# Optimization experiments

Hardware: AMD Instinct MI355X
Metric: run time of the kernel (lower is better)

The kernel has to match this reference:

```python
import jax, jax.numpy as jnp
import numpy as np

N_NODES = 50000
N_EDGES = 800000
HID = 64
OUT = 64
REL = 5


def setup_inputs() -> dict:
    key = jax.random.key(0)
    ks = jax.random.split(key, 9)
    s_in = 1.0 / np.sqrt(HID)
    return {
        "contagion_risk": jax.random.normal(ks[0], (N_NODES, HID), jnp.float32),
        "edge_weight": jax.random.uniform(ks[1], (N_EDGES,), jnp.float32),
        # torch Linear weights stored transposed as [in, out] so y = x @ W + b
        "W_in_w": jax.random.uniform(ks[2], (HID, HID), jnp.float32, -s_in, s_in),
        "W_in_b": jax.random.uniform(ks[3], (HID,), jnp.float32, -s_in, s_in),
        "W_rel": jax.random.uniform(ks[4], (REL, HID, HID), jnp.float32, -s_in, s_in),
        "W_out_w": jax.random.uniform(ks[5], (HID, OUT), jnp.float32, -s_in, s_in),
        "W_out_b": jax.random.uniform(ks[6], (OUT,), jnp.float32, -s_in, s_in),
        "edge_index": jax.random.randint(ks[7], (2, N_EDGES), 0, N_NODES, jnp.int64 if jax.config.jax_enable_x64 else jnp.int32),
        "edge_type": jax.random.randint(ks[8], (N_EDGES,), 0, REL, jnp.int32),
        "num_nodes": N_NODES,
    }


def _dan_forward(contagion_risk, W_in_w, W_in_b, W_rel, W_out_w, W_out_b,
                 edge_index, edge_type, num_nodes):
    row, col = edge_index[0], edge_index[1]  # dst, src
    x = contagion_risk @ W_in_w + W_in_b                       # [N, H]
    x_j = x[col]                                               # [E, H] gather

    # gcn_norm (no self loops, unit edge weights): deg over col
    ones = jnp.ones(col.shape[0], x.dtype)
    deg = jax.ops.segment_sum(ones, col, num_segments=num_nodes)
    dis = jnp.where(deg > 0, jax.lax.rsqrt(jnp.maximum(deg, 1.0)), 0.0)
    norm_w = (dis[row] * dis[col])[:, None]                    # [E, 1]
    msg_gcn = jax.ops.segment_sum(x_j * norm_w, row, num_segments=num_nodes)

    # per-relation masked GEMM (grouped GEMM over REL relation types)
    res = jnp.zeros_like(x_j)
    for i in range(W_rel.shape[0]):
        mask = (edge_type == i)[:, None]
        res = res + jnp.where(mask, x_j @ W_rel[i], 0.0)

    # segment softmax over destination-node groups (per feature channel)
    seg_max = jax.ops.segment_max(res, row, num_segments=num_nodes)
    e = jnp.exp(res - seg_max[row])
    seg_sum = jax.ops.segment_sum(e, row, num_segments=num_nodes)
    weig = e / (seg_sum[row] + 1e-16)

    msg = jax.ops.segment_sum(res * weig, row, num_segments=num_nodes)
    out = (msg_gcn + 0.5 * jax.nn.relu(msg)) @ W_out_w + W_out_b
    return out


def reference(contagion_risk, edge_weight, W_in_w, W_in_b, W_rel, W_out_w, W_out_b,
              edge_index, edge_type, num_nodes):
    # edge_weight is accepted by the original forward but never used
    return _dan_forward(contagion_risk, W_in_w, W_in_b, W_rel, W_out_w, W_out_b,
                        edge_index, edge_type, num_nodes)
```

## Files before the change

kernel.cpp:

```cpp
#include <hip/hip_runtime.h>
#include <hip/hip_bf16.h>

#define HID 64
#define REL 5
#define EPB 4096
#define BKT 256

typedef short bf16x8 __attribute__((ext_vector_type(8)));
typedef float f32x4 __attribute__((ext_vector_type(4)));

__device__ __forceinline__ float bf2f(unsigned short u) {
    return __uint_as_float(((unsigned)u) << 16);
}
__device__ __forceinline__ unsigned short f2bf(float f) {
    __hip_bfloat16 h = (__hip_bfloat16)f;
    return *(unsigned short*)&h;
}
__device__ __forceinline__ void dec_edge(const int* __restrict__ ei, int i64,
                                         int E, int e, int& r, int& c) {
    if (i64) { r = ei[2 * e]; c = ei[2 * (E + e)]; }
    else     { r = ei[e];     c = ei[E + e]; }
}

__global__ void k_detect(const unsigned short* __restrict__ wb,
                         const int* __restrict__ ei, int* flags) {
    int lane = threadIdx.x;
    bool big = (lane < 32) ? (fabsf(bf2f(wb[2 * lane])) > 0.26f) : false;
    unsigned long long b1 = __ballot(big);
    bool odd_nz = (ei[2 * lane + 1] != 0);
    unsigned long long b2 = __ballot(odd_nz);
    if (lane == 0) {
        flags[0] = (b1 != 0ull) ? 1 : 0;
        flags[1] = (b2 == 0ull) ? 1 : 0;
    }
}

__global__ void k_pack(const void* Win, const void* bin, const void* Wr,
                       const void* Wout, const void* bout,
                       unsigned short* __restrict__ Bpk,
                       float* __restrict__ binf, float* __restrict__ boutf,
                       const int* __restrict__ flags) {
    int f = flags[0];
    int gid = blockIdx.x * 256 + threadIdx.x;
    if (gid < 7 * 2 * 4 * 64) {
        int lane = gid & 63;
        int nt = (gid >> 6) & 3;
        int ks = (gid >> 8) & 1;
        int mat = gid >> 9;
        int q = lane >> 4, n = nt * 16 + (lane & 15);
#pragma unroll
        for (int j = 0; j < 8; j++) {
            int k = ks * 32 + q * 8 + j;
            int idx = k * 64 + n;
            float val;
            if (mat == 0)
                val = f ? ((const float*)Win)[idx] : bf2f(((const unsigned short*)Win)[idx]);
            else if (mat <= 5) {
                int ii = (mat - 1) * 4096 + idx;
                val = f ? ((const float*)Wr)[ii] : bf2f(((const unsigned short*)Wr)[ii]);
            } else
                val = f ? ((const float*)Wout)[idx] : bf2f(((const unsigned short*)Wout)[idx]);
            Bpk[(size_t)gid * 8 + j] = f2bf(val);
        }
    }
    if (gid < 64)
        binf[gid] = f ? ((const float*)bin)[gid] : bf2f(((const unsigned short*)bin)[gid]);
    else if (gid >= 64 && gid < 128) {
        int i = gid - 64;
        boutf[i] = f ? ((const float*)bout)[i] : bf2f(((const unsigned short*)bout)[i]);
    }
}

__global__ void k_p1a(const int* __restrict__ ei, const int* __restrict__ flags,
                      int* __restrict__ hist, int E, int NB, int nblk) {
    extern __shared__ int lh[];
    int tid = threadIdx.x, blk = blockIdx.x;
    for (int i = tid; i < 2 * NB; i += 256) lh[i] = 0;
    __syncthreads();
    int i64 = flags[1];
#pragma unroll
    for (int k = 0; k < EPB / 256; k++) {
        int e = blk * EPB + k * 256 + tid;
        if (e < E) {
            int r, c;
            dec_edge(ei, i64, E, e, r, c);
            atomicAdd(&lh[r >> 8], 1);
            atomicAdd(&lh[NB + (c >> 8)], 1);
        }
    }
    __syncthreads();
    int NBn = NB * nblk;
    for (int i = tid; i < NB; i += 256) {
        hist[i * nblk + blk] = lh[i];
        hist[NBn + i * nblk + blk] = lh[NB + i];
    }
}

__global__ void s_blk(const int* __restrict__ v, int* __restrict__ bsum, int M) {
    __shared__ int red[256];
    int t = threadIdx.x;
    int i0 = blockIdx.x * 1024 + t * 4;
    int s = 0;
#pragma unroll
    for (int j = 0; j < 4; j++) { int i = i0 + j; if (i < M) s += v[i]; }
    red[t] = s;
    __syncthreads();
    for (int d = 128; d > 0; d >>= 1) {
        if (t < d) red[t] += red[t + d];
        __syncthreads();
    }
    if (t == 0) bsum[blockIdx.x] = red[0];
}

__global__ void s_top(int* __restrict__ bsum, int nsb) {
    __shared__ int v[1024];
    int t = threadIdx.x;
    for (int i = t; i < nsb; i += 256) v[i] = bsum[i];
    __syncthreads();
    if (t == 0) {
        int run = 0;
        for (int i = 0; i < nsb; i++) { int x = v[i]; v[i] = run; run += x; }
    }
    __syncthreads();
    for (int i = t; i < nsb; i += 256) bsum[i] = v[i];
}

__global__ void s_apply(int* __restrict__ v, const int* __restrict__ bsum, int M) {
    __shared__ int red[256];
    int t = threadIdx.x;
    int i0 = blockIdx.x * 1024 + t * 4;
    int x[4];
    int s = 0;
#pragma unroll
    for (int j = 0; j < 4; j++) {
        int i = i0 + j;
        x[j] = (i < M) ? v[i] : 0;
        s += x[j];
    }
    red[t] = s;
    __syncthreads();
    for (int d = 1; d < 256; d <<= 1) {
        int add = (t >= d) ? red[t - d] : 0;
        __syncthreads();
        red[t] += add;
        __syncthreads();
    }
    int run = bsum[blockIdx.x] + red[t] - s;
#pragma unroll
    for (int j = 0; j < 4; j++) {
        int i = i0 + j;
        if (i < M) { int tmp = x[j]; v[i] = run; run += tmp; }
    }
}

__global__ void k_p1c(const int* __restrict__ ei, const int* __restrict__ et,
                      const int* __restrict__ flags, const int* __restrict__ hist,
                      unsigned* __restrict__ rbuf, unsigned char* __restrict__ cb8,
                      int E, int NB, int nblk) {
    extern __shared__ int lh[];
    int tid = threadIdx.x, blk = blockIdx.x;
    for (int i = tid; i < 2 * NB; i += 256) lh[i] = 0;
    __syncthreads();
    int i64 = flags[1];
    int NBn = NB * nblk;
#pragma unroll
    for (int k = 0; k < EPB / 256; k++) {
        int e = blk * EPB + k * 256 + tid;
        if (e < E) {
            int r, c;
            dec_edge(ei, i64, E, e, r, c);
            int t = et[e];
            int binR = r >> 8;
            int posR = hist[binR * nblk + blk] + atomicAdd(&lh[binR], 1);
            rbuf[posR] = ((unsigned)(r & 255) << 20) | ((unsigned)t << 17) | (unsigned)c;
            int binC = c >> 8;
            int posC = hist[NBn + binC * nblk + blk] - E + atomicAdd(&lh[NB + binC], 1);
            cb8[posC] = (unsigned char)(c & 255);
        }
    }
}

__global__ void k_p2(const unsigned* __restrict__ rbuf, const unsigned char* __restrict__ cb8,
                     const int* __restrict__ hist,
                     int* __restrict__ off, unsigned* __restrict__ edata4,
                     float* __restrict__ dis, int E, int N, int NB, int nblk) {
    __shared__ int lcnt[BKT], excl[BKT], lcnt2[BKT];
    int tid = threadIdx.x;
    int bk = blockIdx.x;
    if (bk < NB) {
        int bstart = hist[bk * nblk];
        int bend = (bk + 1 < NB) ? hist[(bk + 1) * nblk] : E;
        lcnt[tid] = 0; lcnt2[tid] = 0;
        __syncthreads();
        for (int e = bstart + tid; e < bend; e += 256)
            atomicAdd(&lcnt[(rbuf[e] >> 20) & 255], 1);
        __syncthreads();
        int s = lcnt[tid];
        excl[tid] = s;
        __syncthreads();
        for (int d = 1; d < 256; d <<= 1) {
            int add = (tid >= d) ? excl[tid - d] : 0;
            __syncthreads();
            excl[tid] += add;
            __syncthreads();
        }
        int base = excl[tid] - s;
        excl[tid] = base;
        __syncthreads();
        int node = bk * BKT + tid;
        if (node < N) off[node] = bstart + base;
        if (bk == 0 && tid == 0) off[N] = E;
        for (int e = bstart + tid; e < bend; e += 256) {
            unsigned rec = rbuf[e];
            int rl = (rec >> 20) & 255;
            int t = (rec >> 17) & 7;
            int c = rec & 0x1FFFF;
            int pos = bstart + excl[rl] + atomicAdd(&lcnt2[rl], 1);
            edata4[pos] = (unsigned)c | ((unsigned)t << 20);
        }
    } else {
        int bk2 = bk - NB;
        int NBn = NB * nblk;
        int cstart = hist[NBn + bk2 * nblk] - E;
        int cend = (bk2 + 1 < NB) ? hist[NBn + (bk2 + 1) * nblk] - E : E;
        lcnt[tid] = 0;
        __syncthreads();
        for (int e = cstart + tid; e < cend; e += 256)
            atomicAdd(&lcnt[cb8[e]], 1);
        __syncthreads();
        int node = bk2 * BKT + tid;
        int d = lcnt[tid];
        dis[node] = (d > 0) ? rsqrtf((float)d) : 0.f;
    }
}

__device__ __forceinline__ bf16x8 load_a8(const void* A, int f, size_t base) {
    if (f) {
        const float* Af = (const float*)A + base;
        bf16x8 r;
#pragma unroll
        for (int j = 0; j < 8; j++) r[j] = (short)f2bf(Af[j]);
        return r;
    }
    return *(const bf16x8*)((const unsigned short*)A + base);
}

__global__ void __launch_bounds__(256)
k_xy(const void* __restrict__ A, const unsigned short* __restrict__ Bpk,
     const float* __restrict__ binf, const float* __restrict__ dis,
     unsigned short* __restrict__ Yi, const int* __restrict__ flags,
     int N, int Np) {
    __shared__ unsigned short Bs[6 * 2 * 4 * 64 * 8];
    __shared__ unsigned short Xs[64 * 64];
    __shared__ unsigned short Xss[64 * 64];
    __shared__ unsigned short Ys[64 * 64];
    __shared__ float bs[64];
    int tid = threadIdx.x;
    for (int i = tid; i < 6 * 2 * 4 * 64; i += 256)
        ((uint4*)Bs)[i] = ((const uint4*)Bpk)[i];
    if (tid < 64) bs[tid] = binf[tid];
    __syncthreads();

    int w = tid >> 6, lane = tid & 63;
    int q = lane >> 4, n16 = lane & 15;
    int mrow = w * 16 + n16;
    int f = flags[0];
    int arow = min(blockIdx.x * 64 + mrow, N - 1);
    bf16x8 a0 = load_a8(A, f, (size_t)arow * 64 + 8 * q);
    bf16x8 a1 = load_a8(A, f, (size_t)arow * 64 + 8 * q + 32);

    float disv[4];
#pragma unroll
    for (int r = 0; r < 4; r++) {
        int node = blockIdx.x * 64 + w * 16 + 4 * q + r;
        disv[r] = dis[node];
    }

    size_t snode = (size_t)(blockIdx.x * 64 + mrow);

#pragma unroll
    for (int nt = 0; nt < 4; nt++) {
        f32x4 d = {0.f, 0.f, 0.f, 0.f};
        bf16x8 b0 = *(const bf16x8*)(Bs + (size_t)(((0 * 2 + 0) * 4 + nt) * 64 + lane) * 8);
        bf16x8 b1 = *(const bf16x8*)(Bs + (size_t)(((0 * 2 + 1) * 4 + nt) * 64 + lane) * 8);
        d = __builtin_amdgcn_mfma_f32_16x16x32_bf16(a0, b0, d, 0, 0, 0);
        d = __builtin_amdgcn_mfma_f32_16x16x32_bf16(a1, b1, d, 0, 0, 0);
        int col = nt * 16 + n16;
#pragma unroll
        for (int r = 0; r < 4; r++) {
            int rowl = w * 16 + 4 * q + r;
            float xval = d[r] + bs[col];
            Xs[rowl * 64 + col] = f2bf(xval);
            Xss[rowl * 64 + col] = f2bf(xval * disv[r]);
        }
    }
    bf16x8 a20 = *(const bf16x8*)(Xs + mrow * 64 + 8 * q);
    bf16x8 a21 = *(const bf16x8*)(Xs + mrow * 64 + 8 * q + 32);

    for (int rel = 0; rel < REL; rel++) {
        int mat = 1 + rel;
#pragma unroll
        for (int nt = 0; nt < 4; nt++) {
            f32x4 d = {0.f, 0.f, 0.f, 0.f};
            bf16x8 b0 = *(const bf16x8*)(Bs + (size_t)(((mat * 2 + 0) * 4 + nt) * 64 + lane) * 8);
            bf16x8 b1 = *(const bf16x8*)(Bs + (size_t)(((mat * 2 + 1) * 4 + nt) * 64 + lane) * 8);
            d = __builtin_amdgcn_mfma_f32_16x16x32_bf16(a20, b0, d, 0, 0, 0);
            d = __builtin_amdgcn_mfma_f32_16x16x32_bf16(a21, b1, d, 0, 0, 0);
            int col = nt * 16 + n16;
#pragma unroll
            for (int r = 0; r < 4; r++)
                Ys[(w * 16 + 4 * q + r) * 64 + col] = f2bf(d[r]);
        }
        unsigned short* dst = Yi + ((size_t)rel * Np + snode) * 128;
#pragma unroll
        for (int ch = 0; ch < 2; ch++) {
            int c0 = 8 * q + 32 * ch;
            bf16x8 y8 = *(const bf16x8*)(Ys + mrow * 64 + c0);
            bf16x8 x8 = *(const bf16x8*)(Xss + mrow * 64 + c0);
            bf16x8 lo, hi;
#pragma unroll
            for (int j = 0; j < 4; j++) {
                lo[2 * j] = y8[j];     lo[2 * j + 1] = x8[j];
                hi[2 * j] = y8[4 + j]; hi[2 * j + 1] = x8[4 + j];
            }
            *(bf16x8*)(dst + 2 * c0)     = lo;
            *(bf16x8*)(dst + 2 * c0 + 8) = hi;
        }
    }
}

__global__ void __launch_bounds__(256)
k_main(const unsigned short* __restrict__ Yi, const int* __restrict__ off,
       const unsigned* __restrict__ edata4, const float* __restrict__ dis,
       unsigned short* __restrict__ v, int N, int Np) {
    int tid = threadIdx.x;
    int wv = tid >> 6, lane = tid & 63;
    int n = blockIdx.x * 4 + wv;
    if (n >= N) return;
    int half = lane >> 5;
    int co = (lane & 31) * 4;
    int e0 = off[n], e1 = off[n + 1];
    float s0 = 0.f, s1 = 0.f, u0 = 0.f, u1 = 0.f, g0 = 0.f, g1 = 0.f;
    float s0b = 0.f, s1b = 0.f, u0b = 0.f, u1b = 0.f, g0b = 0.f, g1b = 0.f;

    int e = e0 + half;
    for (; e + 2 < e1; e += 4) {
        unsigned mda = edata4[e];
        unsigned mdb = edata4[e + 2];
        int ca = mda & 0xFFFFF, ta = mda >> 20;
        int cb = mdb & 0xFFFFF, tb = mdb >> 20;
        uint2 ya = *(const uint2*)(Yi + ((size_t)ta * Np + ca) * 128 + co);
        uint2 yb = *(const uint2*)(Yi + ((size_t)tb * Np + cb) * 128 + co);
        float r0 = __uint_as_float(ya.x << 16);
        float r1 = __uint_as_float(ya.y << 16);
        g0 += __uint_as_float(ya.x & 0xFFFF0000u);
        g1 += __uint_as_float(ya.y & 0xFFFF0000u);
        float p0 = __expf(fminf(r0, 60.f));
        float p1 = __expf(fminf(r1, 60.f));
        s0 += p0; s1 += p1;
        u0 += r0 * p0; u1 += r1 * p1;
        float r0b = __uint_as_float(yb.x << 16);
        float r1b = __uint_as_float(yb.y << 16);
        g0b += __uint_as_float(yb.x & 0xFFFF0000u);
        g1b += __uint_as_float(yb.y & 0xFFFF0000u);
        float p0b = __expf(fminf(r0b, 60.f));
        float p1b = __expf(fminf(r1b, 60.f));
        s0b += p0b; s1b += p1b;
        u0b += r0b * p0b; u1b += r1b * p1b;
    }
    if (e < e1) {
        unsigned md = edata4[e];
        int c = md & 0xFFFFF, t = md >> 20;
        uint2 ya = *(const uint2*)(Yi + ((size_t)t * Np + c) * 128 + co);
        float r0 = __uint_as_float(ya.x << 16);
        float r1 = __uint_as_float(ya.y << 16);
        g0 += __uint_as_float(ya.x & 0xFFFF0000u);
        g1 += __uint_as_float(ya.y & 0xFFFF0000u);
        float p0 = __expf(fminf(r0, 60.f));
        float p1 = __expf(fminf(r1, 60.f));
        s0 += p0; s1 += p1;
        u0 += r0 * p0; u1 += r1 * p1;
    }
    s0 += s0b; s1 += s1b; u0 += u0b; u1 += u1b; g0 += g0b; g1 += g1b;

    s0 += __shfl_xor(s0, 32); s1 += __shfl_xor(s1, 32);
    u0 += __shfl_xor(u0, 32); u1 += __shfl_xor(u1, 32);
    g0 += __shfl_xor(g0, 32); g1 += __shfl_xor(g1, 32);
    if (half == 0) {
        float dn = dis[n];
        float m0 = u0 / (s0 + 1e-16f), m1 = u1 / (s1 + 1e-16f);
        float v0 = g0 * dn + 0.5f * fmaxf(m0, 0.f);
        float v1 = g1 * dn + 0.5f * fmaxf(m1, 0.f);
        unsigned pack = (unsigned)f2bf(v0) | ((unsigned)f2bf(v1) << 16);
        *(unsigned*)(v + (size_t)n * 64 + (lane & 31) * 2) = pack;
    }
}

__global__ void __launch_bounds__(256)
k_out(const unsigned short* __restrict__ v, const unsigned short* __restrict__ Bpk,
      const float* __restrict__ boutf, void* __restrict__ outv,
      const int* __restrict__ flags, int N, int Np) {
    __shared__ unsigned short Bs[2 * 4 * 64 * 8];
    __shared__ float Os[64 * 64];
    __shared__ float bs[64];
    int tid = threadIdx.x;
    const unsigned short* src = Bpk + (size_t)6 * 2 * 4 * 64 * 8;
    for (int i = tid; i < 2 * 4 * 64; i += 256)
        ((uint4*)Bs)[i] = ((const uint4*)src)[i];
    if (tid < 64) bs[tid] = boutf[tid];
    __syncthreads();

    int w = tid >> 6, lane = tid & 63;
    int q = lane >> 4, n16 = lane & 15;
    int mrow = w * 16 + n16;
    int arow = min(blockIdx.x * 64 + mrow, N - 1);
    bf16x8 a0 = *(const bf16x8*)(v + (size_t)arow * 64 + 8 * q);
    bf16x8 a1 = *(const bf16x8*)(v + (size_t)arow * 64 + 8 * q + 32);
    int f = flags[0];
#pragma unroll
    for (int nt = 0; nt < 4; nt++) {
        f32x4 d = {0.f, 0.f, 0.f, 0.f};
        bf16x8 b0 = *(const bf16x8*)(Bs + (size_t)((0 * 4 + nt) * 64 + lane) * 8);
        bf16x8 b1 = *(const bf16x8*)(Bs + (size_t)((1 * 4 + nt) * 64 + lane) * 8);
        d = __builtin_amdgcn_mfma_f32_16x16x32_bf16(a0, b0, d, 0, 0, 0);
        d = __builtin_amdgcn_mfma_f32_16x16x32_bf16(a1, b1, d, 0, 0, 0);
        int col = nt * 16 + n16;
#pragma unroll
        for (int r = 0; r < 4; r++)
            Os[(w * 16 + 4 * q + r) * 64 + col] = d[r] + bs[col];
    }
    int node = blockIdx.x * 64 + mrow;
    if (node < N) {
        if (f) {
            float* dst = (float*)outv + (size_t)node * 64;
#pragma unroll
            for (int cchunk = 0; cchunk < 2; cchunk++) {
                int c0 = 8 * q + 32 * cchunk;
                *(f32x4*)(dst + c0)     = *(const f32x4*)(Os + mrow * 64 + c0);
                *(f32x4*)(dst + c0 + 4) = *(const f32x4*)(Os + mrow * 64 + c0 + 4);
            }
        } else {
            unsigned short* dst = (unsigned short*)outv + (size_t)node * 64;
#pragma unroll
            for (int cchunk = 0; cchunk < 2; cchunk++) {
                int c0 = 8 * q + 32 * cchunk;
                bf16x8 pk;
#pragma unroll
                for (int j = 0; j < 8; j++)
                    pk[j] = (short)f2bf(Os[mrow * 64 + c0 + j]);
                *(bf16x8*)(dst + c0) = pk;
            }
        }
    }
}

extern "C" void kernel_launch(void* const* d_in, const int* in_sizes, int n_in,
                              void* d_out, int out_size, void* d_ws, size_t ws_size,
                              hipStream_t stream) {
    const void* A    = d_in[0];
    const void* Win  = d_in[2];
    const void* bin  = d_in[3];
    const void* Wrel = d_in[4];
    const void* Wout = d_in[5];
    const void* bout = d_in[6];
    const int* ei = (const int*)d_in[7];
    const int* et = (const int*)d_in[8];
    int N = in_sizes[0] / HID;
    int E = in_sizes[8];
    int Np = ((N + BKT - 1) / BKT) * BKT;
    int NB = Np / BKT;
    int nblk = (E + EPB - 1) / EPB;
    int M = 2 * NB * nblk;
    int nsb = (M + 1023) / 1024;

    char* p = (char*)d_ws;
    auto carve = [&](size_t bytes) {
        char* q = p;
        p += (bytes + 15) & ~(size_t)15;
        return q;
    };
    unsigned short* Yi   = (unsigned short*)carve((size_t)REL * Np * 128 * 2);
    unsigned short* vv   = (unsigned short*)carve((size_t)Np * 64 * 2);
    unsigned*       rbuf = (unsigned*)carve((size_t)E * 4);
    unsigned char*  cb8  = (unsigned char*)carve((size_t)E);
    unsigned*       edata4 = (unsigned*)carve((size_t)E * 4);
    int*            hist = (int*)carve((size_t)M * 4);
    unsigned short* Bpk  = (unsigned short*)carve((size_t)7 * 4096 * 2);
    float* binf  = (float*)carve(64 * 4);
    float* boutf = (float*)carve(64 * 4);
    int* off     = (int*)carve((size_t)(N + 1) * 4);
    float* dis   = (float*)carve((size_t)Np * 4);
    int* bsum    = (int*)carve((size_t)nsb * 4);
    int* flags   = (int*)carve(16);

    size_t lds_part = (size_t)2 * NB * 4;

    k_detect<<<1, 64, 0, stream>>>((const unsigned short*)bin, ei, flags);
    k_pack<<<14, 256, 0, stream>>>(Win, bin, Wrel, Wout, bout, Bpk, binf, boutf, flags);
    k_p1a<<<nblk, 256, lds_part, stream>>>(ei, flags, hist, E, NB, nblk);
    s_blk<<<nsb, 256, 0, stream>>>(hist, bsum, M);
    s_top<<<1, 256, 0, stream>>>(bsum, nsb);
    s_apply<<<nsb, 256, 0, stream>>>(hist, bsum, M);
    k_p1c<<<nblk, 256, lds_part, stream>>>(ei, et, flags, hist, rbuf, cb8, E, NB, nblk);
    k_p2<<<2 * NB, 256, 0, stream>>>(rbuf, cb8, hist, off, edata4, dis, E, N, NB, nblk);
    k_xy<<<Np / 64, 256, 0, stream>>>(A, Bpk, binf, dis, Yi, flags, N, Np);
    k_main<<<(N + 3) / 4, 256, 0, stream>>>(Yi, off, edata4, dis, vv, N, Np);
    k_out<<<Np / 64, 256, 0, stream>>>(vv, Bpk, boutf, d_out, flags, N, Np);
}
```

Measured before the change: 201.2 us.

## Drop detect and scan-top kernels, inline flag detection, unroll gather loop deeper

Removes the standalone k_detect kernel by having each kernel recompute the dtype and index-width flags with a wavefront ballot. Removes the single-block s_top scan by having each s_apply block reduce the preceding block sums itself. Also widens the edge-gather loop in k_main to issue four Yi loads before consuming them, to get more memory requests in flight. Together these cut two serial launches at the cost of redundant tiny reads in every block.

```diff
diff --git a/kernel.cpp b/kernel.cpp
--- a/kernel.cpp
+++ b/kernel.cpp
@@ -16,31 +16,27 @@
     __hip_bfloat16 h = (__hip_bfloat16)f;
     return *(unsigned short*)&h;
 }
+__device__ __forceinline__ int det_f32(const unsigned short* __restrict__ wb) {
+    int lane = threadIdx.x & 63;
+    bool big = (lane < 32) ? (fabsf(bf2f(wb[2 * lane])) > 0.26f) : false;
+    return (__ballot(big) != 0ull) ? 1 : 0;
+}
+__device__ __forceinline__ int det_i64(const int* __restrict__ ei) {
+    int lane = threadIdx.x & 63;
+    bool odd_nz = (ei[2 * lane + 1] != 0);
+    return (__ballot(odd_nz) == 0ull) ? 1 : 0;
+}
 __device__ __forceinline__ void dec_edge(const int* __restrict__ ei, int i64,
                                          int E, int e, int& r, int& c) {
     if (i64) { r = ei[2 * e]; c = ei[2 * (E + e)]; }
     else     { r = ei[e];     c = ei[E + e]; }
 }
 
-__global__ void k_detect(const unsigned short* __restrict__ wb,
-                         const int* __restrict__ ei, int* flags) {
-    int lane = threadIdx.x;
-    bool big = (lane < 32) ? (fabsf(bf2f(wb[2 * lane])) > 0.26f) : false;
-    unsigned long long b1 = __ballot(big);
-    bool odd_nz = (ei[2 * lane + 1] != 0);
-    unsigned long long b2 = __ballot(odd_nz);
-    if (lane == 0) {
-        flags[0] = (b1 != 0ull) ? 1 : 0;
-        flags[1] = (b2 == 0ull) ? 1 : 0;
-    }
-}
-
 __global__ void k_pack(const void* Win, const void* bin, const void* Wr,
                        const void* Wout, const void* bout,
                        unsigned short* __restrict__ Bpk,
-                       float* __restrict__ binf, float* __restrict__ boutf,
-                       const int* __restrict__ flags) {
-    int f = flags[0];
+                       float* __restrict__ binf, float* __restrict__ boutf) {
+    int f = det_f32((const unsigned short*)bin);
     int gid = blockIdx.x * 256 + threadIdx.x;
     if (gid < 7 * 2 * 4 * 64) {
         int lane = gid & 63;
@@ -71,13 +67,13 @@
     }
 }
 
-__global__ void k_p1a(const int* __restrict__ ei, const int* __restrict__ flags,
+__global__ void k_p1a(const int* __restrict__ ei,
                       int* __restrict__ hist, int E, int NB, int nblk) {
     extern __shared__ int lh[];
+    int i64 = det_i64(ei);
     int tid = threadIdx.x, blk = blockIdx.x;
     for (int i = tid; i < 2 * NB; i += 256) lh[i] = 0;
     __syncthreads();
-    int i64 = flags[1];
 #pragma unroll
     for (int k = 0; k < EPB / 256; k++) {
         int e = blk * EPB + k * 256 + tid;
@@ -112,23 +108,22 @@
     if (t == 0) bsum[blockIdx.x] = red[0];
 }
 
-__global__ void s_top(int* __restrict__ bsum, int nsb) {
-    __shared__ int v[1024];
-    int t = threadIdx.x;
-    for (int i = t; i < nsb; i += 256) v[i] = bsum[i];
-    __syncthreads();
-    if (t == 0) {
-        int run = 0;
-        for (int i = 0; i < nsb; i++) { int x = v[i]; v[i] = run; run += x; }
-    }
-    __syncthreads();
-    for (int i = t; i < nsb; i += 256) bsum[i] = v[i];
-}
-
-__global__ void s_apply(int* __restrict__ v, const int* __restrict__ bsum, int M) {
+__global__ void s_apply(int* __restrict__ v, const int* __restrict__ bsum,
+                        int M, int nsb) {
     __shared__ int red[256];
-    int t = threadIdx.x;
-    int i0 = blockIdx.x * 1024 + t * 4;
+    int t = threadIdx.x, bk = blockIdx.x;
+    int acc = 0;
+    for (int i = t; i < nsb; i += 256)
+        if (i < bk) acc += bsum[i];
+    red[t] = acc;
+    __syncthreads();
+    for (int d = 128; d > 0; d >>= 1) {
+        if (t < d) red[t] += red[t + d];
+        __syncthreads();
+    }
+    int base = red[0];
+    __syncthreads();
+    int i0 = bk * 1024 + t * 4;
     int x[4];
     int s = 0;
 #pragma unroll
@@ -145,7 +140,7 @@
         red[t] += add;
         __syncthreads();
     }
-    int run = bsum[blockIdx.x] + red[t] - s;
+    int run = base + red[t] - s;
 #pragma unroll
     for (int j = 0; j < 4; j++) {
         int i = i0 + j;
@@ -154,14 +149,14 @@
 }
 
 __global__ void k_p1c(const int* __restrict__ ei, const int* __restrict__ et,
-                      const int* __restrict__ flags, const int* __restrict__ hist,
+                      const int* __restrict__ hist,
                       unsigned* __restrict__ rbuf, unsigned char* __restrict__ cb8,
                       int E, int NB, int nblk) {
     extern __shared__ int lh[];
+    int i64 = det_i64(ei);
     int tid = threadIdx.x, blk = blockIdx.x;
     for (int i = tid; i < 2 * NB; i += 256) lh[i] = 0;
     __syncthreads();
-    int i64 = flags[1];
     int NBn = NB * nblk;
 #pragma unroll
     for (int k = 0; k < EPB / 256; k++) {
@@ -246,15 +241,16 @@
 }
 
 __global__ void __launch_bounds__(256)
-k_xy(const void* __restrict__ A, const unsigned short* __restrict__ Bpk,
+k_xy(const void* __restrict__ A, const void* __restrict__ binp,
+     const unsigned short* __restrict__ Bpk,
      const float* __restrict__ binf, const float* __restrict__ dis,
-     unsigned short* __restrict__ Yi, const int* __restrict__ flags,
-     int N, int Np) {
+     unsigned short* __restrict__ Yi, int N, int Np) {
     __shared__ unsigned short Bs[6 * 2 * 4 * 64 * 8];
     __shared__ unsigned short Xs[64 * 64];
     __shared__ unsigned short Xss[64 * 64];
     __shared__ unsigned short Ys[64 * 64];
     __shared__ float bs[64];
+    int f = det_f32((const unsigned short*)binp);
     int tid = threadIdx.x;
     for (int i = tid; i < 6 * 2 * 4 * 64; i += 256)
         ((uint4*)Bs)[i] = ((const uint4*)Bpk)[i];
@@ -264,7 +260,6 @@
     int w = tid >> 6, lane = tid & 63;
     int q = lane >> 4, n16 = lane & 15;
     int mrow = w * 16 + n16;
-    int f = flags[0];
     int arow = min(blockIdx.x * 64 + mrow, N - 1);
     bf16x8 a0 = load_a8(A, f, (size_t)arow * 64 + 8 * q);
     bf16x8 a1 = load_a8(A, f, (size_t)arow * 64 + 8 * q + 32);
@@ -344,31 +339,36 @@
     float s0b = 0.f, s1b = 0.f, u0b = 0.f, u1b = 0.f, g0b = 0.f, g1b = 0.f;
 
     int e = e0 + half;
-    for (; e + 2 < e1; e += 4) {
-        unsigned mda = edata4[e];
-        unsigned mdb = edata4[e + 2];
-        int ca = mda & 0xFFFFF, ta = mda >> 20;
-        int cb = mdb & 0xFFFFF, tb = mdb >> 20;
-        uint2 ya = *(const uint2*)(Yi + ((size_t)ta * Np + ca) * 128 + co);
-        uint2 yb = *(const uint2*)(Yi + ((size_t)tb * Np + cb) * 128 + co);
-        float r0 = __uint_as_float(ya.x << 16);
-        float r1 = __uint_as_float(ya.y << 16);
-        g0 += __uint_as_float(ya.x & 0xFFFF0000u);
-        g1 += __uint_as_float(ya.y & 0xFFFF0000u);
-        float p0 = __expf(fminf(r0, 60.f));
-        float p1 = __expf(fminf(r1, 60.f));
-        s0 += p0; s1 += p1;
-        u0 += r0 * p0; u1 += r1 * p1;
-        float r0b = __uint_as_float(yb.x << 16);
-        float r1b = __uint_as_float(yb.y << 16);
-        g0b += __uint_as_float(yb.x & 0xFFFF0000u);
-        g1b += __uint_as_float(yb.y & 0xFFFF0000u);
-        float p0b = __expf(fminf(r0b, 60.f));
-        float p1b = __expf(fminf(r1b, 60.f));
-        s0b += p0b; s1b += p1b;
-        u0b += r0b * p0b; u1b += r1b * p1b;
-    }
-    if (e < e1) {
+    for (; e + 6 < e1; e += 8) {
+        unsigned md[4];
+#pragma unroll
+        for (int j = 0; j < 4; j++) md[j] = edata4[e + 2 * j];
+        uint2 y[4];
+#pragma unroll
+        for (int j = 0; j < 4; j++) {
+            int c = md[j] & 0xFFFFF, t = md[j] >> 20;
+            y[j] = *(const uint2*)(Yi + ((size_t)t * Np + c) * 128 + co);
+        }
+#pragma unroll
+        for (int j = 0; j < 4; j++) {
+            float r0 = __uint_as_float(y[j].x << 16);
+            float r1 = __uint_as_float(y[j].y << 16);
+            float p0 = __expf(fminf(r0, 60.f));
+            float p1 = __expf(fminf(r1, 60.f));
+            if (j & 1) {
+                g0b += __uint_as_float(y[j].x & 0xFFFF0000u);
+                g1b += __uint_as_float(y[j].y & 0xFFFF0000u);
+                s0b += p0; s1b += p1;
+                u0b += r0 * p0; u1b += r1 * p1;
+            } else {
+                g0 += __uint_as_float(y[j].x & 0xFFFF0000u);
+                g1 += __uint_as_float(y[j].y & 0xFFFF0000u);
+                s0 += p0; s1 += p1;
+                u0 += r0 * p0; u1 += r1 * p1;
+            }
+        }
+    }
+    for (; e < e1; e += 2) {
         unsigned md = edata4[e];
         int c = md & 0xFFFFF, t = md >> 20;
         uint2 ya = *(const uint2*)(Yi + ((size_t)t * Np + c) * 128 + co);
@@ -397,12 +397,13 @@
 }
 
 __global__ void __launch_bounds__(256)
-k_out(const unsigned short* __restrict__ v, const unsigned short* __restrict__ Bpk,
-      const float* __restrict__ boutf, void* __restrict__ outv,
-      const int* __restrict__ flags, int N, int Np) {
+k_out(const unsigned short* __restrict__ v, const void* __restrict__ binp,
+      const unsigned short* __restrict__ Bpk,
+      const float* __restrict__ boutf, void* __restrict__ outv, int N, int Np) {
     __shared__ unsigned short Bs[2 * 4 * 64 * 8];
     __shared__ float Os[64 * 64];
     __shared__ float bs[64];
+    int f = det_f32((const unsigned short*)binp);
     int tid = threadIdx.x;
     const unsigned short* src = Bpk + (size_t)6 * 2 * 4 * 64 * 8;
     for (int i = tid; i < 2 * 4 * 64; i += 256)
@@ -416,7 +417,6 @@
     int arow = min(blockIdx.x * 64 + mrow, N - 1);
     bf16x8 a0 = *(const bf16x8*)(v + (size_t)arow * 64 + 8 * q);
     bf16x8 a1 = *(const bf16x8*)(v + (size_t)arow * 64 + 8 * q + 32);
-    int f = flags[0];
 #pragma unroll
     for (int nt = 0; nt < 4; nt++) {
         f32x4 d = {0.f, 0.f, 0.f, 0.f};
@@ -491,19 +491,16 @@
     int* off     = (int*)carve((size_t)(N + 1) * 4);
     float* dis   = (float*)carve((size_t)Np * 4);
     int* bsum    = (int*)carve((size_t)nsb * 4);
-    int* flags   = (int*)carve(16);
 
     size_t lds_part = (size_t)2 * NB * 4;
 
-    k_detect<<<1, 64, 0, stream>>>((const unsigned short*)bin, ei, flags);
-    k_pack<<<14, 256, 0, stream>>>(Win, bin, Wrel, Wout, bout, Bpk, binf, boutf, flags);
-    k_p1a<<<nblk, 256, lds_part, stream>>>(ei, flags, hist, E, NB, nblk);
+    k_pack<<<14, 256, 0, stream>>>(Win, bin, Wrel, Wout, bout, Bpk, binf, boutf);
+    k_p1a<<<nblk, 256, lds_part, stream>>>(ei, hist, E, NB, nblk);
     s_blk<<<nsb, 256, 0, stream>>>(hist, bsum, M);
-    s_top<<<1, 256, 0, stream>>>(bsum, nsb);
-    s_apply<<<nsb, 256, 0, stream>>>(hist, bsum, M);
-    k_p1c<<<nblk, 256, lds_part, stream>>>(ei, et, flags, hist, rbuf, cb8, E, NB, nblk);
+    s_apply<<<nsb, 256, 0, stream>>>(hist, bsum, M, nsb);
+    k_p1c<<<nblk, 256, lds_part, stream>>>(ei, et, hist, rbuf, cb8, E, NB, nblk);
     k_p2<<<2 * NB, 256, 0, stream>>>(rbuf, cb8, hist, off, edata4, dis, E, N, NB, nblk);
-    k_xy<<<Np / 64, 256, 0, stream>>>(A, Bpk, binf, dis, Yi, flags, N, Np);
+    k_xy<<<Np / 64, 256, 0, stream>>>(A, bin, Bpk, binf, dis, Yi, N, Np);
     k_main<<<(N + 3) / 4, 256, 0, stream>>>(Yi, off, edata4, dis, vv, N, Np);
-    k_out<<<Np / 64, 256, 0, stream>>>(vv, Bpk, boutf, d_out, flags, N, Np);
-}
+    k_out<<<Np / 64, 256, 0, stream>>>(vv, bin, Bpk, boutf, d_out, N, Np);
+}
```

New measurement: 194.9 us. 1.03x faster.
